# Performance work log

Measured on AMD Instinct MI355X. Metric: run time of the kernel, lower is better.

## Reference

```python
import jax, jax.numpy as jnp
import numpy as np

S, B, H, T = 512, 64, 512, 32

def setup_inputs() -> dict:
    key = jax.random.key(0)
    ks = jax.random.split(key, 6)
    hidden = jax.random.normal(ks[0], (S, B, H), jnp.float32)
    lens = jax.random.randint(ks[1], (B,), 1, S + 1)  # sentence lengths in [1, S]
    masks = jnp.ones((S, B), jnp.bool_)  # unused (attention is None), kept for signature parity
    W1 = jax.random.normal(ks[2], (H, H), jnp.float32) / np.sqrt(H)
    b1 = jnp.zeros((H,), jnp.float32)
    W2 = jax.random.normal(ks[3], (H, T), jnp.float32) / np.sqrt(H)
    b2 = jnp.zeros((T,), jnp.float32)
    # xavier_normal_ init for transition
    transition = jax.random.normal(ks[4], (T, T), jnp.float32) * np.sqrt(2.0 / (T + T))
    return {"hidden": hidden, "lens": lens, "masks": masks,
            "W1": W1, "b1": b1, "W2": W2, "b2": b2, "transition": transition}


def _viterbi(emissions, lens, transition):
    # emissions: [S, B, T]; transition[curr, prev]
    Sdim, Bdim, Tn = emissions.shape
    ident = jnp.broadcast_to(jnp.arange(Tn), (Bdim, Tn))  # identity backpointers for padded steps

    def step(fv, inp):
        em_t, t = inp
        scores = fv[:, None, :] + transition[None, :, :]  # [B, curr, prev]
        bp = jnp.argmax(scores, axis=-1)                  # [B, T]
        new_fv = jnp.max(scores, axis=-1) + em_t          # [B, T]
        active = (t < lens)[:, None]
        fv = jnp.where(active, new_fv, fv)                # freeze state past sentence end
        bp = jnp.where(active, bp, ident)
        return fv, bp

    fv0 = emissions[0]
    ts = jnp.arange(1, Sdim)
    fv, bps = jax.lax.scan(step, fv0, (emissions[1:], ts))  # bps: [S-1, B, T]
    best_id = jnp.argmax(fv, axis=-1)   # [B]
    best_score = jnp.max(fv, axis=-1)   # [B]

    def back(tag, bp_t):
        prev = jnp.take_along_axis(bp_t, tag[:, None], axis=1)[:, 0]
        return prev, prev

    _, prevs = jax.lax.scan(back, best_id, bps, reverse=True)  # [S-1, B]
    paths = jnp.concatenate([prevs, best_id[None]], axis=0)    # [S, B]; beyond len-1 the tag repeats
    return paths, best_score


def reference(hidden, lens, masks, W1, b1, W2, b2, transition):
    # hidden2emission: Linear -> Sigmoid -> Linear
    h1 = jax.nn.sigmoid(hidden @ W1 + b1)   # [S, B, H]
    emissions = h1 @ W2 + b2                # [S, B, T]
    paths, best_score = _viterbi(emissions, lens, transition)
    return paths, best_score
```

## Files before the change

### kernel.cpp

```cpp
#include <hip/hip_runtime.h>
#include <math.h>

#define SDIM 512
#define BDIM 64
#define HDIM 512
#define TDIM 32
#define MTOT (SDIM * BDIM)

typedef __attribute__((ext_vector_type(8))) short bf16x8;
typedef __attribute__((ext_vector_type(4))) float f32x4;

__device__ unsigned short g_w1hT[HDIM * HDIM];
__device__ unsigned short g_w1lT[HDIM * HDIM];
__device__ unsigned short g_w2hT[TDIM * HDIM];
__device__ unsigned short g_w2lT[TDIM * HDIM];
__device__ float g_em[(size_t)MTOT * TDIM];

__device__ __forceinline__ unsigned short f2bf(float x) {
  union { float f; unsigned int u; } v; v.f = x;
  unsigned int r = v.u + 0x7FFFu + ((v.u >> 16) & 1u);
  return (unsigned short)(r >> 16);
}
__device__ __forceinline__ float bf2f(unsigned short h) {
  union { float f; unsigned int u; } v; v.u = ((unsigned int)h) << 16; return v.f;
}
__device__ __forceinline__ float readlane_f(float v, int l) {
  return __int_as_float(__builtin_amdgcn_readlane(__float_as_int(v), l));
}

__global__ void split_kernel(const float* __restrict__ W1, const float* __restrict__ W2) {
  const int n = blockIdx.x;
  const int k0 = threadIdx.x * 4;
  if (n < HDIM) {
    ushort4 h, l; float x;
    x = W1[(size_t)(k0 + 0) * HDIM + n]; h.x = f2bf(x); l.x = f2bf(x - bf2f(h.x));
    x = W1[(size_t)(k0 + 1) * HDIM + n]; h.y = f2bf(x); l.y = f2bf(x - bf2f(h.y));
    x = W1[(size_t)(k0 + 2) * HDIM + n]; h.z = f2bf(x); l.z = f2bf(x - bf2f(h.z));
    x = W1[(size_t)(k0 + 3) * HDIM + n]; h.w = f2bf(x); l.w = f2bf(x - bf2f(h.w));
    *(ushort4*)&g_w1hT[(size_t)n * HDIM + k0] = h;
    *(ushort4*)&g_w1lT[(size_t)n * HDIM + k0] = l;
  } else {
    const int t = n - HDIM;
    ushort4 h, l; float x;
    x = W2[(size_t)(k0 + 0) * TDIM + t]; h.x = f2bf(x); l.x = f2bf(x - bf2f(h.x));
    x = W2[(size_t)(k0 + 1) * TDIM + t]; h.y = f2bf(x); l.y = f2bf(x - bf2f(h.y));
    x = W2[(size_t)(k0 + 2) * TDIM + t]; h.z = f2bf(x); l.z = f2bf(x - bf2f(h.z));
    x = W2[(size_t)(k0 + 3) * TDIM + t]; h.w = f2bf(x); l.w = f2bf(x - bf2f(h.w));
    *(ushort4*)&g_w2hT[(size_t)t * HDIM + k0] = h;
    *(ushort4*)&g_w2lT[(size_t)t * HDIM + k0] = l;
  }
}

__global__ __launch_bounds__(256) void emis_kernel(
    const float* __restrict__ hidden, const float* __restrict__ b1,
    const float* __restrict__ b2)
{
  __shared__ unsigned short lAh[64][40];
  __shared__ unsigned short lAl[64][40];
  __shared__ unsigned short lBh[128][40];
  __shared__ unsigned short lBl[128][40];
  __shared__ unsigned short H1h[64][136];
  __shared__ unsigned short H1l[64][136];

  const int tid = threadIdx.x;
  const int s = blockIdx.x;
  const int row0 = s * 64;
  const int wave = tid >> 6;
  const int lane = tid & 63;
  const int l15 = lane & 15;
  const int l4 = lane >> 4;
  const int wr1 = (wave >> 1) * 32;
  const int wc1 = (wave & 1) * 64;

  f32x4 acc_em[2];
  acc_em[0] = (f32x4)(0.f);
  acc_em[1] = (f32x4)(0.f);

  for (int jcb = 0; jcb < 4; ++jcb) {
    const int jc = jcb * 128;

    f32x4 acc1[2][4];
#pragma unroll
    for (int i = 0; i < 2; ++i)
#pragma unroll
      for (int j = 0; j < 4; ++j) acc1[i][j] = (f32x4)(0.f);

    for (int k0 = 0; k0 < HDIM; k0 += 32) {
#pragma unroll
      for (int i = 0; i < 2; ++i) {
        int f4 = tid + 256 * i;
        int r = f4 >> 3, q = f4 & 7;
        float4 v = *(const float4*)&hidden[(size_t)(row0 + r) * HDIM + k0 + 4 * q];
        ushort4 h, l;
        h.x = f2bf(v.x); l.x = f2bf(v.x - bf2f(h.x));
        h.y = f2bf(v.y); l.y = f2bf(v.y - bf2f(h.y));
        h.z = f2bf(v.z); l.z = f2bf(v.z - bf2f(h.z));
        h.w = f2bf(v.w); l.w = f2bf(v.w - bf2f(h.w));
        *(ushort4*)&lAh[r][4 * q] = h;
        *(ushort4*)&lAl[r][4 * q] = l;
      }
#pragma unroll
      for (int i = 0; i < 2; ++i) {
        int f8 = tid + 256 * i;
        int nl = f8 >> 2, kq8 = f8 & 3;
        *(uint4*)&lBh[nl][8 * kq8] =
            *(const uint4*)&g_w1hT[(size_t)(jc + nl) * HDIM + k0 + 8 * kq8];
        *(uint4*)&lBl[nl][8 * kq8] =
            *(const uint4*)&g_w1lT[(size_t)(jc + nl) * HDIM + k0 + 8 * kq8];
      }
      __syncthreads();

      bf16x8 aH[2], aL[2];
#pragma unroll
      for (int i = 0; i < 2; ++i) {
        aH[i] = *(const bf16x8*)&lAh[wr1 + 16 * i + l15][8 * l4];
        aL[i] = *(const bf16x8*)&lAl[wr1 + 16 * i + l15][8 * l4];
      }
#pragma unroll
      for (int j = 0; j < 4; ++j) {
        bf16x8 bH = *(const bf16x8*)&lBh[wc1 + 16 * j + l15][8 * l4];
        bf16x8 bL = *(const bf16x8*)&lBl[wc1 + 16 * j + l15][8 * l4];
#pragma unroll
        for (int i = 0; i < 2; ++i) {
          acc1[i][j] = __builtin_amdgcn_mfma_f32_16x16x32_bf16(aH[i], bH, acc1[i][j], 0, 0, 0);
          acc1[i][j] = __builtin_amdgcn_mfma_f32_16x16x32_bf16(aH[i], bL, acc1[i][j], 0, 0, 0);
          acc1[i][j] = __builtin_amdgcn_mfma_f32_16x16x32_bf16(aL[i], bH, acc1[i][j], 0, 0, 0);
        }
      }
      __syncthreads();
    }

#pragma unroll
    for (int j = 0; j < 4; ++j) {
      const int col = wc1 + 16 * j + l15;
      const float bv = b1[jc + col];
#pragma unroll
      for (int i = 0; i < 2; ++i) {
#pragma unroll
        for (int r = 0; r < 4; ++r) {
          int lrow = wr1 + 16 * i + 4 * l4 + r;
          float h = 1.f / (1.f + expf(-(acc1[i][j][r] + bv)));
          unsigned short hh = f2bf(h);
          unsigned short hl = f2bf(h - bf2f(hh));
          H1h[lrow][col] = hh;
          H1l[lrow][col] = hl;
        }
      }
    }
    __syncthreads();

#pragma unroll
    for (int ks = 0; ks < 4; ++ks) {
      bf16x8 aH2 = *(const bf16x8*)&H1h[16 * wave + l15][32 * ks + 8 * l4];
      bf16x8 aL2 = *(const bf16x8*)&H1l[16 * wave + l15][32 * ks + 8 * l4];
#pragma unroll
      for (int j2 = 0; j2 < 2; ++j2) {
        const size_t wo = (size_t)(16 * j2 + l15) * HDIM + jc + 32 * ks + 8 * l4;
        bf16x8 bH2 = *(const bf16x8*)&g_w2hT[wo];
        bf16x8 bL2 = *(const bf16x8*)&g_w2lT[wo];
        acc_em[j2] = __builtin_amdgcn_mfma_f32_16x16x32_bf16(aH2, bH2, acc_em[j2], 0, 0, 0);
        acc_em[j2] = __builtin_amdgcn_mfma_f32_16x16x32_bf16(aH2, bL2, acc_em[j2], 0, 0, 0);
        acc_em[j2] = __builtin_amdgcn_mfma_f32_16x16x32_bf16(aL2, bH2, acc_em[j2], 0, 0, 0);
      }
    }
    __syncthreads();
  }

#pragma unroll
  for (int j2 = 0; j2 < 2; ++j2) {
    const int t = 16 * j2 + l15;
    const float bv = b2[t];
#pragma unroll
    for (int r = 0; r < 4; ++r) {
      int b = 16 * wave + 4 * l4 + r;
      g_em[((size_t)b * SDIM + s) * TDIM + t] = acc_em[j2][r] + bv;
    }
  }
}

__global__ __launch_bounds__(64) void viterbi_kernel(
    const int* __restrict__ lens, const float* __restrict__ trans,
    float* __restrict__ out)
{
  __shared__ unsigned int bps32[SDIM / 4][TDIM];
  const int b = blockIdx.x;
  const int lane = threadIdx.x;
  const int c = lane & 31;

  float tr[TDIM];
#pragma unroll
  for (int p = 0; p < TDIM; p += 4) {
    float4 t4 = *(const float4*)&trans[c * TDIM + p];
    tr[p] = t4.x; tr[p + 1] = t4.y; tr[p + 2] = t4.z; tr[p + 3] = t4.w;
  }

  int len;
  { const int* p32 = lens;
    len = (p32[1] == 0) ? (int)((const long long*)lens)[b] : p32[b]; }

  const float* emc = g_em + (size_t)b * SDIM * TDIM + c;

  float fvown = emc[0];
  float sfv[TDIM];
#pragma unroll
  for (int p = 0; p < TDIM; ++p) sfv[p] = readlane_f(fvown, p);

  float ebuf[12];
#pragma unroll
  for (int j = 0; j < 12; ++j) ebuf[j] = emc[(size_t)(1 + j) * TDIM];

  unsigned int bpk = 0u;

#define VSTEP(T, PH, EV)                                                       \
  {                                                                            \
    float sv[TDIM];                                                            \
    _Pragma("unroll")                                                          \
    for (int p = 0; p < TDIM; ++p) sv[p] = sfv[p] + tr[p];                     \
    float v16[16]; int i16[16];                                                \
    _Pragma("unroll")                                                          \
    for (int p = 0; p < 16; ++p) {                                             \
      bool g = sv[2 * p] >= sv[2 * p + 1];                                     \
      v16[p] = g ? sv[2 * p] : sv[2 * p + 1];                                  \
      i16[p] = g ? 2 * p : 2 * p + 1;                                          \
    }                                                                          \
    float v8[8]; int i8[8];                                                    \
    _Pragma("unroll")                                                          \
    for (int p = 0; p < 8; ++p) {                                              \
      bool g = v16[2 * p] >= v16[2 * p + 1];                                   \
      v8[p] = g ? v16[2 * p] : v16[2 * p + 1];                                 \
      i8[p] = g ? i16[2 * p] : i16[2 * p + 1];                                 \
    }                                                                          \
    float v4[4]; int i4[4];                                                    \
    _Pragma("unroll")                                                          \
    for (int p = 0; p < 4; ++p) {                                              \
      bool g = v8[2 * p] >= v8[2 * p + 1];                                     \
      v4[p] = g ? v8[2 * p] : v8[2 * p + 1];                                   \
      i4[p] = g ? i8[2 * p] : i8[2 * p + 1];                                   \
    }                                                                          \
    bool ga = v4[0] >= v4[1];                                                  \
    float va = ga ? v4[0] : v4[1]; int ia = ga ? i4[0] : i4[1];                \
    bool gb = v4[2] >= v4[3];                                                  \
    float vb = gb ? v4[2] : v4[3]; int ib = gb ? i4[2] : i4[3];                \
    bool gf = va >= vb;                                                        \
    float m0 = gf ? va : vb; int i0 = gf ? ia : ib;                            \
    const bool act = (T) < len;                                                \
    fvown = act ? (m0 + (EV)) : fvown;                                         \
    int bp = act ? i0 : c;                                                     \
    _Pragma("unroll")                                                          \
    for (int p = 0; p < TDIM; ++p) sfv[p] = readlane_f(fvown, p);              \
    bpk |= (unsigned)bp << (8 * (PH));                                         \
    if ((PH) == 3) { bps32[(T) >> 2][c] = bpk; bpk = 0u; }                     \
  }

#define LOADQ(BASE, T0)                                                        \
  {                                                                            \
    _Pragma("unroll")                                                          \
    for (int j = 0; j < 4; ++j) {                                              \
      int lt = (T0) + j; lt = lt > (SDIM - 1) ? (SDIM - 1) : lt;               \
      ebuf[(BASE) + j] = emc[(size_t)lt * TDIM];                               \
    }                                                                          \
  }

  {
    int tq = 1;
    for (; tq <= SDIM - 19; tq += 12) {
      VSTEP(tq + 0, 1, ebuf[0]) VSTEP(tq + 1, 2, ebuf[1])
      VSTEP(tq + 2, 3, ebuf[2]) VSTEP(tq + 3, 0, ebuf[3])
      LOADQ(0, tq + 12)
      VSTEP(tq + 4, 1, ebuf[4]) VSTEP(tq + 5, 2, ebuf[5])
      VSTEP(tq + 6, 3, ebuf[6]) VSTEP(tq + 7, 0, ebuf[7])
      LOADQ(4, tq + 16)
      VSTEP(tq + 8, 1, ebuf[8]) VSTEP(tq + 9, 2, ebuf[9])
      VSTEP(tq + 10, 3, ebuf[10]) VSTEP(tq + 11, 0, ebuf[11])
      LOADQ(8, tq + 20)
    }
    VSTEP(505, 1, ebuf[0]) VSTEP(506, 2, ebuf[1]) VSTEP(507, 3, ebuf[2])
    VSTEP(508, 0, ebuf[3]) VSTEP(509, 1, ebuf[4]) VSTEP(510, 2, ebuf[5])
    VSTEP(511, 3, ebuf[6])
  }
#undef VSTEP
#undef LOADQ

  float bs = fvown;
  int bi = c;
#pragma unroll
  for (int off = 16; off > 0; off >>= 1) {
    float os = __shfl_down(bs, off, 32);
    int oi = __shfl_down(bi, off, 32);
    if (os > bs || (os == bs && oi < bi)) { bs = os; bi = oi; }
  }
  bs = __shfl(bs, 0, 32);
  int tag = __shfl(bi, 0, 32);

  out[(size_t)SDIM * BDIM + b] = bs;
  out[(size_t)(SDIM - 1) * BDIM + b] = (float)tag;

  unsigned bw_next = bps32[SDIM / 4 - 1][c];
  for (int w = SDIM / 4 - 1; w >= 0; --w) {
    unsigned bw = bw_next;
    if (w > 0) bw_next = bps32[w - 1][c];
#pragma unroll
    for (int j = 3; j >= 0; --j) {
      int t = 4 * w + j;
      if (t < 1) continue;
      unsigned word = (unsigned)__builtin_amdgcn_readlane((int)bw, tag);
      tag = (int)((word >> (8 * j)) & 255u);
      out[(size_t)(t - 1) * BDIM + b] = (float)tag;
    }
  }
}

static int find_by_size(const int* in_sizes, int n_in, int sz, int fb) {
  for (int i = 0; i < n_in; ++i) if (in_sizes[i] == sz) return i;
  return fb;
}

extern "C" void kernel_launch(void* const* d_in, const int* in_sizes, int n_in,
                              void* d_out, int out_size, void* d_ws, size_t ws_size,
                              hipStream_t stream) {
  const int i_hidden = find_by_size(in_sizes, n_in, SDIM * BDIM * HDIM, 0);
  const int i_lens   = find_by_size(in_sizes, n_in, BDIM, 1);
  const int i_W1     = find_by_size(in_sizes, n_in, HDIM * HDIM, 3);
  const int i_b1     = find_by_size(in_sizes, n_in, HDIM, 4);
  const int i_W2     = find_by_size(in_sizes, n_in, HDIM * TDIM, 5);
  const int i_b2     = find_by_size(in_sizes, n_in, TDIM, 6);
  const int i_tr     = find_by_size(in_sizes, n_in, TDIM * TDIM, 7);

  const float* hidden = (const float*)d_in[i_hidden];
  const int*   lens   = (const int*)d_in[i_lens];
  const float* W1     = (const float*)d_in[i_W1];
  const float* b1     = (const float*)d_in[i_b1];
  const float* W2     = (const float*)d_in[i_W2];
  const float* b2     = (const float*)d_in[i_b2];
  const float* trans  = (const float*)d_in[i_tr];
  float* out = (float*)d_out;

  split_kernel<<<HDIM + TDIM, 128, 0, stream>>>(W1, W2);
  emis_kernel<<<SDIM, 256, 0, stream>>>(hidden, b1, b2);
  viterbi_kernel<<<BDIM, 64, 0, stream>>>(lens, trans, out);
}
```

Baseline: 275.9 us.

## Split Viterbi max over both wave halves and broadcast state via LDS

The Viterbi step previously had lanes 32-63 duplicate lanes 0-31, with each lane reducing all 32 predecessors after 32 readlane broadcasts. Now each half-wave handles 16 predecessors, reads the forward vector from LDS with float4 loads, reduces with max3 trees, and combines the halves with a cross-half shuffle. The argmax is recovered afterwards by equality matching against the final max. This cuts the scalar readlane and compare/select chain per step, but puts an LDS round trip and two shuffles on the serial critical path. There is no barrier around the LDS write and read, which relies on single-wave lockstep execution.

```diff
diff --git a/kernel.cpp b/kernel.cpp
--- a/kernel.cpp
+++ b/kernel.cpp
@@ -24,8 +24,11 @@
 __device__ __forceinline__ float bf2f(unsigned short h) {
   union { float f; unsigned int u; } v; v.u = ((unsigned int)h) << 16; return v.f;
 }
-__device__ __forceinline__ float readlane_f(float v, int l) {
-  return __int_as_float(__builtin_amdgcn_readlane(__float_as_int(v), l));
+__device__ __forceinline__ float fmax3(float a, float b, float c) {
+  return fmaxf(fmaxf(a, b), c);
+}
+__device__ __forceinline__ int imin3(int a, int b, int c) {
+  int m = a < b ? a : b; return m < c ? m : c;
 }
 
 __global__ void split_kernel(const float* __restrict__ W1, const float* __restrict__ W2) {
@@ -182,16 +185,19 @@
     const int* __restrict__ lens, const float* __restrict__ trans,
     float* __restrict__ out)
 {
+  __shared__ float fvL[64];
   __shared__ unsigned int bps32[SDIM / 4][TDIM];
   const int b = blockIdx.x;
   const int lane = threadIdx.x;
   const int c = lane & 31;
-
-  float tr[TDIM];
-#pragma unroll
-  for (int p = 0; p < TDIM; p += 4) {
-    float4 t4 = *(const float4*)&trans[c * TDIM + p];
-    tr[p] = t4.x; tr[p + 1] = t4.y; tr[p + 2] = t4.z; tr[p + 3] = t4.w;
+  const int h = lane >> 5;
+  const int p0 = 16 * h;
+
+  float tr[16];
+#pragma unroll
+  for (int j = 0; j < 16; j += 4) {
+    float4 t4 = *(const float4*)&trans[c * TDIM + p0 + j];
+    tr[j] = t4.x; tr[j + 1] = t4.y; tr[j + 2] = t4.z; tr[j + 3] = t4.w;
   }
 
   int len;
@@ -201,9 +207,7 @@
   const float* emc = g_em + (size_t)b * SDIM * TDIM + c;
 
   float fvown = emc[0];
-  float sfv[TDIM];
-#pragma unroll
-  for (int p = 0; p < TDIM; ++p) sfv[p] = readlane_f(fvown, p);
+  fvL[lane] = fvown;
 
   float ebuf[12];
 #pragma unroll
@@ -213,41 +217,43 @@
 
 #define VSTEP(T, PH, EV)                                                       \
   {                                                                            \
-    float sv[TDIM];                                                            \
-    _Pragma("unroll")                                                          \
-    for (int p = 0; p < TDIM; ++p) sv[p] = sfv[p] + tr[p];                     \
-    float v16[16]; int i16[16];                                                \
-    _Pragma("unroll")                                                          \
-    for (int p = 0; p < 16; ++p) {                                             \
-      bool g = sv[2 * p] >= sv[2 * p + 1];                                     \
-      v16[p] = g ? sv[2 * p] : sv[2 * p + 1];                                  \
-      i16[p] = g ? 2 * p : 2 * p + 1;                                          \
-    }                                                                          \
-    float v8[8]; int i8[8];                                                    \
-    _Pragma("unroll")                                                          \
-    for (int p = 0; p < 8; ++p) {                                              \
-      bool g = v16[2 * p] >= v16[2 * p + 1];                                   \
-      v8[p] = g ? v16[2 * p] : v16[2 * p + 1];                                 \
-      i8[p] = g ? i16[2 * p] : i16[2 * p + 1];                                 \
-    }                                                                          \
-    float v4[4]; int i4[4];                                                    \
-    _Pragma("unroll")                                                          \
-    for (int p = 0; p < 4; ++p) {                                              \
-      bool g = v8[2 * p] >= v8[2 * p + 1];                                     \
-      v4[p] = g ? v8[2 * p] : v8[2 * p + 1];                                   \
-      i4[p] = g ? i8[2 * p] : i8[2 * p + 1];                                   \
-    }                                                                          \
-    bool ga = v4[0] >= v4[1];                                                  \
-    float va = ga ? v4[0] : v4[1]; int ia = ga ? i4[0] : i4[1];                \
-    bool gb = v4[2] >= v4[3];                                                  \
-    float vb = gb ? v4[2] : v4[3]; int ib = gb ? i4[2] : i4[3];                \
-    bool gf = va >= vb;                                                        \
-    float m0 = gf ? va : vb; int i0 = gf ? ia : ib;                            \
+    float4 q0 = *(const float4*)&fvL[p0];                                      \
+    float4 q1 = *(const float4*)&fvL[p0 + 4];                                  \
+    float4 q2 = *(const float4*)&fvL[p0 + 8];                                  \
+    float4 q3 = *(const float4*)&fvL[p0 + 12];                                 \
+    float sv[16];                                                              \
+    sv[0] = q0.x + tr[0];  sv[1] = q0.y + tr[1];                               \
+    sv[2] = q0.z + tr[2];  sv[3] = q0.w + tr[3];                               \
+    sv[4] = q1.x + tr[4];  sv[5] = q1.y + tr[5];                               \
+    sv[6] = q1.z + tr[6];  sv[7] = q1.w + tr[7];                               \
+    sv[8] = q2.x + tr[8];  sv[9] = q2.y + tr[9];                               \
+    sv[10] = q2.z + tr[10]; sv[11] = q2.w + tr[11];                            \
+    sv[12] = q3.x + tr[12]; sv[13] = q3.y + tr[13];                            \
+    sv[14] = q3.z + tr[14]; sv[15] = q3.w + tr[15];                            \
+    float l0 = fmax3(sv[0], sv[1], sv[2]);                                     \
+    float l1 = fmax3(sv[3], sv[4], sv[5]);                                     \
+    float l2 = fmax3(sv[6], sv[7], sv[8]);                                     \
+    float l3 = fmax3(sv[9], sv[10], sv[11]);                                   \
+    float l4 = fmax3(sv[12], sv[13], sv[14]);                                  \
+    float mh = fmaxf(fmax3(l0, l1, l2), fmax3(l3, l4, sv[15]));                \
+    float mo = __shfl_xor(mh, 32, 64);                                         \
+    float m0 = fmaxf(mh, mo);                                                  \
     const bool act = (T) < len;                                                \
     fvown = act ? (m0 + (EV)) : fvown;                                         \
-    int bp = act ? i0 : c;                                                     \
+    fvL[lane] = fvown;       \
+    int i_[16];                                                                \
     _Pragma("unroll")                                                          \
-    for (int p = 0; p < TDIM; ++p) sfv[p] = readlane_f(fvown, p);              \
+    for (int j = 0; j < 16; ++j) i_[j] = (sv[j] == m0) ? j : 63;               \
+    int u0 = imin3(i_[0], i_[1], i_[2]);                                       \
+    int u1 = imin3(i_[3], i_[4], i_[5]);                                       \
+    int u2 = imin3(i_[6], i_[7], i_[8]);                                       \
+    int u3 = imin3(i_[9], i_[10], i_[11]);                                     \
+    int u4 = imin3(i_[12], i_[13], i_[14]);                                    \
+    int jm = imin3(imin3(u0, u1, u2), imin3(u3, u4, i_[15]), 63);              \
+    int gi = (jm == 63) ? 255 : (p0 + jm);                                     \
+    int go = __shfl_xor(gi, 32, 64);                                           \
+    int im = gi < go ? gi : go;                                                \
+    int bp = act ? im : c;                                                     \
     bpk |= (unsigned)bp << (8 * (PH));                                         \
     if ((PH) == 3) { bps32[(T) >> 2][c] = bpk; bpk = 0u; }                     \
   }
```

After: 239.4 us. 1.15x faster.
